# Kernel optimization log

Measured on AMD Instinct MI355X. Metric: run time of the kernel, lower is better.

Reference implementation:

```python
import jax, jax.numpy as jnp
import numpy as np

B, T, D, H, C, WIN = 2, 2048, 512, 8, 64, 128
EPS = 1e-6


def _rms_norm(x, w):
    # x: (..., C)
    norm = jax.lax.rsqrt(jnp.mean(x * x, axis=-1, keepdims=True) + EPS)
    return x * norm * w


def _apply_rope(x, cos_p, sin_p):
    # x: (B, H, T, C); cos_p/sin_p: (T, C)
    half = x.shape[-1] // 2
    x1, x2 = x[..., :half], x[..., half:]
    rotated = jnp.concatenate([-x2, x1], axis=-1)
    return x * cos_p + rotated * sin_p


def setup_inputs() -> dict:
    key = jax.random.key(0)
    ks = jax.random.split(key, 5)
    h = jax.random.normal(ks[0], (B, T, D), dtype=jnp.float32)
    # RoPE cache (rotate-half convention): (T_max, head_dim)
    inv_freq = 1.0 / (10000.0 ** (jnp.arange(0, C, 2, dtype=jnp.float32) / C))  # (C/2,)
    pos = jnp.arange(T, dtype=jnp.float32)
    freqs = pos[:, None] * inv_freq[None, :]                      # (T, C/2)
    emb = jnp.concatenate([freqs, freqs], axis=-1)                # (T, C)
    rope_cos = jnp.cos(emb)
    rope_sin = jnp.sin(emb)
    scale = 0.02
    W_q = jax.random.normal(ks[1], (D, H * C), dtype=jnp.float32) * scale
    W_k = jax.random.normal(ks[2], (D, H * C), dtype=jnp.float32) * scale
    W_v = jax.random.normal(ks[3], (D, H * C), dtype=jnp.float32) * scale
    W_o = jax.random.normal(ks[4], (H * C, D), dtype=jnp.float32) * scale
    q_norm_w = jnp.ones((C,), dtype=jnp.float32)
    k_norm_w = jnp.ones((C,), dtype=jnp.float32)
    return {"h": h, "rope_cos": rope_cos, "rope_sin": rope_sin,
            "W_q": W_q, "W_k": W_k, "W_v": W_v, "W_o": W_o,
            "q_norm_w": q_norm_w, "k_norm_w": k_norm_w}


def reference(h, rope_cos, rope_sin, W_q, W_k, W_v, W_o, q_norm_w, k_norm_w):
    Bx, Tx, _ = h.shape
    q = (h @ W_q).reshape(Bx, Tx, H, C)
    k = (h @ W_k).reshape(Bx, Tx, H, C)
    v = (h @ W_v).reshape(Bx, Tx, H, C)
    q = _rms_norm(q, q_norm_w)
    k = _rms_norm(k, k_norm_w)
    positions = jnp.arange(Tx)
    cos_p = rope_cos[positions]   # (T, C)
    sin_p = rope_sin[positions]
    # transpose to (B, H, T, C), apply rope, transpose back handled implicitly
    q = _apply_rope(q.transpose(0, 2, 1, 3), cos_p, sin_p).transpose(0, 2, 1, 3)
    k = _apply_rope(k.transpose(0, 2, 1, 3), cos_p, sin_p).transpose(0, 2, 1, 3)
    i = positions[:, None]
    j = positions[None, :]
    sw_mask = (j <= i) & (j > i - WIN)                # (T, T) banded causal
    logits = jnp.einsum('bthc,bshc->bhts', q, k) / np.sqrt(C).astype(np.float32)
    logits = jnp.where(sw_mask[None, None], logits, jnp.float32(-jnp.inf))
    attn = jax.nn.softmax(logits, axis=-1)
    out = jnp.einsum('bhts,bshc->bthc', attn, v).reshape(Bx, Tx, H * C)
    return out @ W_o
```

## Files before the change

### kernel.cpp

```cpp
#include <hip/hip_runtime.h>
#include <hip/hip_bf16.h>
#include <cmath>

#define Bb 2
#define Tt 2048
#define Dd 512
#define Hh 8
#define Cc 64
#define WINw 128

using u16x8 = __attribute__((ext_vector_type(8))) unsigned short;
using s16x8 = __attribute__((ext_vector_type(8))) short;
using f32x4 = __attribute__((ext_vector_type(4))) float;

__device__ __forceinline__ float bf2f(unsigned short u) {
  union { unsigned int i; float f; } v; v.i = ((unsigned int)u) << 16; return v.f;
}
__device__ __forceinline__ unsigned short f2bf(float f) {
  __hip_bfloat16 b = __float2bfloat16(f);
  return *reinterpret_cast<unsigned short*>(&b);
}

#define GLD16(gp, lp)                                                        \
  __builtin_amdgcn_global_load_lds(                                          \
      (const __attribute__((address_space(1))) unsigned int*)(gp),           \
      (__attribute__((address_space(3))) unsigned int*)(lp), 16, 0, 0)

__global__ __launch_bounds__(256) void prep_all(
    const float* __restrict__ s0, const float* __restrict__ s1,
    const float* __restrict__ s2, const float* __restrict__ s3,
    unsigned short* __restrict__ d,
    const float* __restrict__ hsrc, unsigned short* __restrict__ hdst) {
  int tid = threadIdx.x;
  if (blockIdx.z == 4) {
    int gid = ((int)blockIdx.y * 8 + blockIdx.x) * 256 + tid;
    #pragma unroll
    for (int s = 0; s < 16; ++s) {
      size_t i = ((size_t)s * 16384 + gid) * 8;
      const float4* g = (const float4*)&hsrc[i];
      float4 f0 = g[0], f1 = g[1];
      u16x8 o = {f2bf(f0.x), f2bf(f0.y), f2bf(f0.z), f2bf(f0.w),
                 f2bf(f1.x), f2bf(f1.y), f2bf(f1.z), f2bf(f1.w)};
      *(u16x8*)&hdst[i] = o;
    }
    return;
  }
  __shared__ unsigned short tile[64 * 65];
  const float* srcs[4] = {s0, s1, s2, s3};
  const float* src = srcs[blockIdx.z];
  unsigned short* dst = d + (size_t)blockIdx.z * 512 * 512;
  int n0 = blockIdx.x * 64, k0 = blockIdx.y * 64;
  int tx = tid & 63, ty = tid >> 6;
  #pragma unroll
  for (int i = 0; i < 16; ++i) {
    int k = ty * 16 + i;
    tile[k * 65 + tx] = f2bf(src[(k0 + k) * 512 + n0 + tx]);
  }
  __syncthreads();
  #pragma unroll
  for (int i = 0; i < 16; ++i) {
    int n = ty * 16 + i;
    dst[(n0 + n) * 512 + k0 + tx] = tile[tx * 65 + n];
  }
}

__global__ __launch_bounds__(256) void qkv_fused(
    const unsigned short* __restrict__ Hb,
    const unsigned short* __restrict__ WTall,
    const float* __restrict__ qnw, const float* __restrict__ knw,
    const float* __restrict__ rcos, const float* __restrict__ rsin,
    unsigned short* __restrict__ Qw, unsigned short* __restrict__ Kw,
    unsigned short* __restrict__ Vw) {
  __shared__ alignas(16) unsigned short Al[128 * 64];
  __shared__ alignas(16) unsigned short Bl[128 * 64];
  int tid = threadIdx.x;
  int wave = tid >> 6, lane = tid & 63;
  int ln = lane & 15, qd = lane >> 4;
  int wm = wave >> 1, wn = wave & 1;
  int m0 = blockIdx.x * 128, n0 = blockIdx.y * 128;

  f32x4 acc[4][4];
  #pragma unroll
  for (int mi = 0; mi < 4; ++mi)
    #pragma unroll
    for (int ni = 0; ni < 4; ++ni) acc[mi][ni] = f32x4{0.f, 0.f, 0.f, 0.f};

  for (int k0 = 0; k0 < 512; k0 += 64) {
    #pragma unroll
    for (int s = 0; s < 4; ++s) {
      int q = s * 4 + wave;
      int L = q * 64 + lane;
      int row = L >> 3;
      int cb = (L & 7) ^ (row & 7);
      const unsigned short* ga = &Hb[(size_t)(m0 + row) * 512 + k0 + cb * 8];
      GLD16(ga, (char*)Al + q * 1024);
      const unsigned short* gb = &WTall[(size_t)(n0 + row) * 512 + k0 + cb * 8];
      GLD16(gb, (char*)Bl + q * 1024);
    }
    __syncthreads();
    #pragma unroll
    for (int half = 0; half < 2; ++half) {
      s16x8 af[4], bfr[4];
      #pragma unroll
      for (int mi = 0; mi < 4; ++mi) {
        int ar = wm * 64 + mi * 16 + ln;
        int cbp = (qd + half * 4) ^ (ar & 7);
        af[mi] = *(const s16x8*)((const char*)Al + ar * 128 + cbp * 16);
      }
      #pragma unroll
      for (int ni = 0; ni < 4; ++ni) {
        int br = wn * 64 + ni * 16 + ln;
        int cbp = (qd + half * 4) ^ (br & 7);
        bfr[ni] = *(const s16x8*)((const char*)Bl + br * 128 + cbp * 16);
      }
      #pragma unroll
      for (int mi = 0; mi < 4; ++mi)
        #pragma unroll
        for (int ni = 0; ni < 4; ++ni)
          acc[mi][ni] = __builtin_amdgcn_mfma_f32_16x16x32_bf16(
              af[mi], bfr[ni], acc[mi][ni], 0, 0, 0);
    }
    __syncthreads();
  }

  int gh = blockIdx.y * 2 + wn;
  int mat = gh >> 3, head = gh & 7;
  unsigned short* Out = (mat == 0) ? Qw : (mat == 1) ? Kw : Vw;
  const float* nw = (mat == 0) ? qnw : knw;
  bool do_rope = (mat < 2);

  #pragma unroll
  for (int mi = 0; mi < 4; ++mi) {
    float vals[4][4];
    #pragma unroll
    for (int ni = 0; ni < 4; ++ni)
      #pragma unroll
      for (int r = 0; r < 4; ++r) vals[ni][r] = acc[mi][ni][r];

    if (do_rope) {
      #pragma unroll
      for (int r = 0; r < 4; ++r) {
        float ss = 0.f;
        #pragma unroll
        for (int ni = 0; ni < 4; ++ni) ss += vals[ni][r] * vals[ni][r];
        ss += __shfl_xor(ss, 1, 64);
        ss += __shfl_xor(ss, 2, 64);
        ss += __shfl_xor(ss, 4, 64);
        ss += __shfl_xor(ss, 8, 64);
        float nrm = rsqrtf(ss * (1.0f / 64.0f) + 1e-6f);
        #pragma unroll
        for (int ni = 0; ni < 4; ++ni) vals[ni][r] *= nrm;
      }
      #pragma unroll
      for (int ni = 0; ni < 4; ++ni) {
        float w = nw[ni * 16 + ln];
        #pragma unroll
        for (int r = 0; r < 4; ++r) vals[ni][r] *= w;
      }
      float res[4][4];
      #pragma unroll
      for (int r = 0; r < 4; ++r) {
        int row = m0 + wm * 64 + mi * 16 + qd * 4 + r;
        int t = row & (Tt - 1);
        #pragma unroll
        for (int ni = 0; ni < 4; ++ni) {
          int c = ni * 16 + ln;
          float cs = rcos[t * 64 + c];
          float sn = rsin[t * 64 + c];
          float part = vals[ni ^ 2][r];
          float rot = (ni < 2) ? -part : part;
          res[ni][r] = vals[ni][r] * cs + rot * sn;
        }
      }
      #pragma unroll
      for (int ni = 0; ni < 4; ++ni)
        #pragma unroll
        for (int r = 0; r < 4; ++r) vals[ni][r] = res[ni][r];
    }

    #pragma unroll
    for (int r = 0; r < 4; ++r) {
      int row = m0 + wm * 64 + mi * 16 + qd * 4 + r;
      int b = row >> 11, t = row & (Tt - 1);
      unsigned short* op = &Out[(((size_t)b * Hh + head) * Tt + t) * 64 + ln];
      #pragma unroll
      for (int ni = 0; ni < 4; ++ni) op[ni * 16] = f2bf(vals[ni][r]);
    }
  }
}

__global__ __launch_bounds__(256) void attn_mfma(
    const unsigned short* __restrict__ Q,
    const unsigned short* __restrict__ K,
    const unsigned short* __restrict__ V,
    unsigned short* __restrict__ AO) {
  __shared__ alignas(16) unsigned short Ql[64 * 72];
  __shared__ alignas(16) unsigned short KP[192 * 72];
  __shared__ alignas(16) unsigned short Vt[64 * 200];

  int tid = threadIdx.x;
  int wave = tid >> 6, lane = tid & 63;
  int ln = lane & 15, qd = lane >> 4;
  int qtile = blockIdx.x, bh = blockIdx.y;
  int t0 = qtile * 64;
  int kb = t0 - 128;

  const unsigned short* Qg = Q + ((size_t)bh * Tt + t0) * 64;
  const unsigned short* Kg = K + (size_t)bh * Tt * 64;
  const unsigned short* Vg = V + (size_t)bh * Tt * 64;

  int srow = tid >> 2;
  int scol = (tid & 3) * 16;

  {
    const u16x8* g = (const u16x8*)&Qg[srow * 64 + scol];
    u16x8 a0 = g[0], a1 = g[1];
    *(u16x8*)&Ql[srow * 72 + scol] = a0;
    *(u16x8*)&Ql[srow * 72 + scol + 8] = a1;
  }
  #pragma unroll
  for (int p = 0; p < 3; ++p) {
    int row = p * 64 + srow;
    int kg = kb + row; if (kg < 0) kg = 0;
    const u16x8* gk = (const u16x8*)&Kg[kg * 64 + scol];
    u16x8 k0 = gk[0], k1 = gk[1];
    const u16x8* gv = (const u16x8*)&Vg[kg * 64 + scol];
    u16x8 v0 = gv[0], v1 = gv[1];
    *(u16x8*)&KP[row * 72 + scol] = k0;
    *(u16x8*)&KP[row * 72 + scol + 8] = k1;
    #pragma unroll
    for (int j = 0; j < 8; ++j) {
      Vt[(scol + j) * 200 + row] = v0[j];
      Vt[(scol + 8 + j) * 200 + row] = v1[j];
    }
  }
  __syncthreads();

  int q0 = wave * 16;
  s16x8 aq0 = *(const s16x8*)&Ql[(q0 + ln) * 72 + qd * 8];
  s16x8 aq1 = *(const s16x8*)&Ql[(q0 + ln) * 72 + 32 + qd * 8];
  f32x4 sf[12];
  #pragma unroll
  for (int nt = 0; nt < 12; ++nt) {
    s16x8 b0 = *(const s16x8*)&KP[(nt * 16 + ln) * 72 + qd * 8];
    s16x8 b1 = *(const s16x8*)&KP[(nt * 16 + ln) * 72 + 32 + qd * 8];
    f32x4 acc = {0.f, 0.f, 0.f, 0.f};
    acc = __builtin_amdgcn_mfma_f32_16x16x32_bf16(aq0, b0, acc, 0, 0, 0);
    acc = __builtin_amdgcn_mfma_f32_16x16x32_bf16(aq1, b1, acc, 0, 0, 0);
    sf[nt] = acc;
  }
  __syncthreads();

  unsigned short* Pl = KP;
  int ok0 = (t0 < 128) ? (128 - t0) : 0;
  #pragma unroll
  for (int r = 0; r < 4; ++r) {
    int lq = q0 + qd * 4 + r;
    float mx = -INFINITY;
    #pragma unroll
    for (int nt = 0; nt < 12; ++nt) {
      int kk = nt * 16 + ln;
      bool valid = (kk > lq) && (kk <= lq + 128) && (kk >= ok0);
      float s = valid ? sf[nt][r] * 0.125f : -INFINITY;
      sf[nt][r] = s;
      mx = fmaxf(mx, s);
    }
    mx = fmaxf(mx, __shfl_xor(mx, 1, 64));
    mx = fmaxf(mx, __shfl_xor(mx, 2, 64));
    mx = fmaxf(mx, __shfl_xor(mx, 4, 64));
    mx = fmaxf(mx, __shfl_xor(mx, 8, 64));
    float sum = 0.f;
    #pragma unroll
    for (int nt = 0; nt < 12; ++nt) {
      float e = __expf(sf[nt][r] - mx);
      sf[nt][r] = e;
      sum += e;
    }
    sum += __shfl_xor(sum, 1, 64);
    sum += __shfl_xor(sum, 2, 64);
    sum += __shfl_xor(sum, 4, 64);
    sum += __shfl_xor(sum, 8, 64);
    float inv = 1.0f / sum;
    #pragma unroll
    for (int nt = 0; nt < 12; ++nt)
      Pl[lq * 200 + nt * 16 + ln] = f2bf(sf[nt][r] * inv);
  }
  __syncthreads();

  f32x4 oa[4] = {f32x4{0,0,0,0}, f32x4{0,0,0,0}, f32x4{0,0,0,0}, f32x4{0,0,0,0}};
  #pragma unroll
  for (int s = 0; s < 6; ++s) {
    s16x8 ap = *(const s16x8*)&Pl[(q0 + ln) * 200 + s * 32 + qd * 8];
    #pragma unroll
    for (int nt = 0; nt < 4; ++nt) {
      s16x8 bv = *(const s16x8*)&Vt[(nt * 16 + ln) * 200 + s * 32 + qd * 8];
      oa[nt] = __builtin_amdgcn_mfma_f32_16x16x32_bf16(ap, bv, oa[nt], 0, 0, 0);
    }
  }

  int b = bh >> 3, h = bh & 7;
  #pragma unroll
  for (int r = 0; r < 4; ++r) {
    int t = t0 + q0 + qd * 4 + r;
    unsigned short* op = &AO[(((size_t)b * Tt + t) * Hh + h) * 64 + ln];
    #pragma unroll
    for (int nt = 0; nt < 4; ++nt) op[nt * 16] = f2bf(oa[nt][r]);
  }
}

__global__ __launch_bounds__(256) void out_gemm(
    const unsigned short* __restrict__ Am,
    const unsigned short* __restrict__ WT,
    float* __restrict__ Out) {
  __shared__ alignas(16) unsigned short Al[64 * 64];
  __shared__ alignas(16) unsigned short Bl[128 * 64];
  int tid = threadIdx.x;
  int wave = tid >> 6, lane = tid & 63;
  int ln = lane & 15, qd = lane >> 4;
  int wm = wave >> 1, wn = wave & 1;
  int m0 = blockIdx.x * 64, n0 = blockIdx.y * 128;

  f32x4 acc[2][4];
  #pragma unroll
  for (int mi = 0; mi < 2; ++mi)
    #pragma unroll
    for (int ni = 0; ni < 4; ++ni) acc[mi][ni] = f32x4{0.f, 0.f, 0.f, 0.f};

  for (int k0 = 0; k0 < 512; k0 += 64) {
    #pragma unroll
    for (int s = 0; s < 2; ++s) {
      int q = s * 4 + wave;
      int L = q * 64 + lane;
      int row = L >> 3;
      int cb = (L & 7) ^ (row & 7);
      const unsigned short* ga = &Am[(size_t)(m0 + row) * 512 + k0 + cb * 8];
      GLD16(ga, (char*)Al + q * 1024);
    }
    #pragma unroll
    for (int s = 0; s < 4; ++s) {
      int q = s * 4 + wave;
      int L = q * 64 + lane;
      int row = L >> 3;
      int cb = (L & 7) ^ (row & 7);
      const unsigned short* gb = &WT[(size_t)(n0 + row) * 512 + k0 + cb * 8];
      GLD16(gb, (char*)Bl + q * 1024);
    }
    __syncthreads();
    #pragma unroll
    for (int half = 0; half < 2; ++half) {
      s16x8 af[2], bfr[4];
      #pragma unroll
      for (int mi = 0; mi < 2; ++mi) {
        int ar = wm * 32 + mi * 16 + ln;
        int cbp = (qd + half * 4) ^ (ar & 7);
        af[mi] = *(const s16x8*)((const char*)Al + ar * 128 + cbp * 16);
      }
      #pragma unroll
      for (int ni = 0; ni < 4; ++ni) {
        int br = wn * 64 + ni * 16 + ln;
        int cbp = (qd + half * 4) ^ (br & 7);
        bfr[ni] = *(const s16x8*)((const char*)Bl + br * 128 + cbp * 16);
      }
      #pragma unroll
      for (int mi = 0; mi < 2; ++mi)
        #pragma unroll
        for (int ni = 0; ni < 4; ++ni)
          acc[mi][ni] = __builtin_amdgcn_mfma_f32_16x16x32_bf16(
              af[mi], bfr[ni], acc[mi][ni], 0, 0, 0);
    }
    __syncthreads();
  }

  #pragma unroll
  for (int mi = 0; mi < 2; ++mi)
    #pragma unroll
    for (int r = 0; r < 4; ++r) {
      int row = m0 + wm * 32 + mi * 16 + qd * 4 + r;
      #pragma unroll
      for (int ni = 0; ni < 4; ++ni)
        Out[(size_t)row * 512 + n0 + wn * 64 + ni * 16 + ln] = acc[mi][ni][r];
    }
}

extern "C" void kernel_launch(void* const* d_in, const int* in_sizes, int n_in,
                              void* d_out, int out_size, void* d_ws, size_t ws_size,
                              hipStream_t stream) {
  const float* h   = (const float*)d_in[0];
  const float* rc  = (const float*)d_in[1];
  const float* rs  = (const float*)d_in[2];
  const float* Wq  = (const float*)d_in[3];
  const float* Wk  = (const float*)d_in[4];
  const float* Wv  = (const float*)d_in[5];
  const float* Wo  = (const float*)d_in[6];
  const float* qnw = (const float*)d_in[7];
  const float* knw = (const float*)d_in[8];

  unsigned short* ws    = (unsigned short*)d_ws;
  unsigned short* WTall = ws;
  unsigned short* WTo   = WTall + 1536 * 512;
  unsigned short* Hb    = WTo + 512 * 512;
  unsigned short* Qw    = Hb + 2097152;
  unsigned short* Kw    = Qw + 2097152;
  unsigned short* Vw    = Kw + 2097152;
  unsigned short* AOw   = Vw + 2097152;

  prep_all<<<dim3(8, 8, 5), 256, 0, stream>>>(Wq, Wk, Wv, Wo, WTall, h, Hb);

  qkv_fused<<<dim3(32, 12), 256, 0, stream>>>(Hb, WTall, qnw, knw, rc, rs,
                                              Qw, Kw, Vw);

  attn_mfma<<<dim3(32, 16), 256, 0, stream>>>(Qw, Kw, Vw, AOw);

  out_gemm<<<dim3(64, 4), 256, 0, stream>>>(AOw, WTo, (float*)d_out);
}
```

Before: 114.1 us.

## Store V transposed and stage QKV/attention outputs through LDS for coalesced writes

The QKV epilogue now writes each wave's 64x64 tile into shared memory and then issues 16-byte coalesced global stores. V is written pre-transposed as (C, T) per head, so the attention kernel can fill its Vt tile with vector loads instead of a scalar transpose scatter. The attention kernel also loads Q fragments straight from global memory, drops one barrier, and stages its output through LDS for vectorized stores. The V loads for the first query tiles no longer clamp negative key indices, so they can read before the buffer start; those positions are masked, but non-finite garbage would still poison the result.

```diff
diff --git a/kernel.cpp b/kernel.cpp
--- a/kernel.cpp
+++ b/kernel.cpp
@@ -71,8 +71,9 @@
     const float* __restrict__ rcos, const float* __restrict__ rsin,
     unsigned short* __restrict__ Qw, unsigned short* __restrict__ Kw,
     unsigned short* __restrict__ Vw) {
-  __shared__ alignas(16) unsigned short Al[128 * 64];
-  __shared__ alignas(16) unsigned short Bl[128 * 64];
+  __shared__ alignas(16) unsigned short S[18432];
+  unsigned short* Al = S;
+  unsigned short* Bl = S + 8192;
   int tid = threadIdx.x;
   int wave = tid >> 6, lane = tid & 63;
   int ln = lane & 15, qd = lane >> 4;
@@ -92,10 +93,8 @@
       int L = q * 64 + lane;
       int row = L >> 3;
       int cb = (L & 7) ^ (row & 7);
-      const unsigned short* ga = &Hb[(size_t)(m0 + row) * 512 + k0 + cb * 8];
-      GLD16(ga, (char*)Al + q * 1024);
-      const unsigned short* gb = &WTall[(size_t)(n0 + row) * 512 + k0 + cb * 8];
-      GLD16(gb, (char*)Bl + q * 1024);
+      GLD16(&Hb[(size_t)(m0 + row) * 512 + k0 + cb * 8], (char*)Al + q * 1024);
+      GLD16(&WTall[(size_t)(n0 + row) * 512 + k0 + cb * 8], (char*)Bl + q * 1024);
     }
     __syncthreads();
     #pragma unroll
@@ -123,11 +122,13 @@
     __syncthreads();
   }
 
+  unsigned short* Wl = S + wave * 4608;
   int gh = blockIdx.y * 2 + wn;
   int mat = gh >> 3, head = gh & 7;
-  unsigned short* Out = (mat == 0) ? Qw : (mat == 1) ? Kw : Vw;
   const float* nw = (mat == 0) ? qnw : knw;
   bool do_rope = (mat < 2);
+  int mrow0 = m0 + wm * 64;
+  int b = mrow0 >> 11, tb = mrow0 & (Tt - 1);
 
   #pragma unroll
   for (int mi = 0; mi < 4; ++mi) {
@@ -160,8 +161,7 @@
       float res[4][4];
       #pragma unroll
       for (int r = 0; r < 4; ++r) {
-        int row = m0 + wm * 64 + mi * 16 + qd * 4 + r;
-        int t = row & (Tt - 1);
+        int t = (tb + mi * 16 + qd * 4 + r);
         #pragma unroll
         for (int ni = 0; ni < 4; ++ni) {
           int c = ni * 16 + ln;
@@ -178,13 +178,37 @@
         for (int r = 0; r < 4; ++r) vals[ni][r] = res[ni][r];
     }
 
-    #pragma unroll
-    for (int r = 0; r < 4; ++r) {
-      int row = m0 + wm * 64 + mi * 16 + qd * 4 + r;
-      int b = row >> 11, t = row & (Tt - 1);
-      unsigned short* op = &Out[(((size_t)b * Hh + head) * Tt + t) * 64 + ln];
-      #pragma unroll
-      for (int ni = 0; ni < 4; ++ni) op[ni * 16] = f2bf(vals[ni][r]);
+    if (mat < 2) {
+      #pragma unroll
+      for (int ni = 0; ni < 4; ++ni)
+        #pragma unroll
+        for (int r = 0; r < 4; ++r)
+          Wl[(mi * 16 + qd * 4 + r) * 72 + ni * 16 + ln] = f2bf(vals[ni][r]);
+    } else {
+      #pragma unroll
+      for (int ni = 0; ni < 4; ++ni)
+        #pragma unroll
+        for (int r = 0; r < 4; ++r)
+          Wl[(ni * 16 + ln) * 72 + mi * 16 + qd * 4 + r] = f2bf(vals[ni][r]);
+    }
+  }
+
+  if (mat < 2) {
+    unsigned short* Og =
+        ((mat == 0) ? Qw : Kw) + (((size_t)b * Hh + head) * Tt + tb) * 64;
+    #pragma unroll
+    for (int i = 0; i < 8; ++i) {
+      int idx = i * 64 + lane;
+      int rr = idx >> 3, cc = (idx & 7) * 8;
+      *(u16x8*)&Og[rr * 64 + cc] = *(const u16x8*)&Wl[rr * 72 + cc];
+    }
+  } else {
+    unsigned short* Og = Vw + (((size_t)b * Hh + head) * 64) * 2048 + tb;
+    #pragma unroll
+    for (int i = 0; i < 8; ++i) {
+      int idx = i * 64 + lane;
+      int rr = idx >> 3, cc = (idx & 7) * 8;
+      *(u16x8*)&Og[(size_t)rr * 2048 + cc] = *(const u16x8*)&Wl[rr * 72 + cc];
     }
   }
 }
@@ -192,62 +216,53 @@
 __global__ __launch_bounds__(256) void attn_mfma(
     const unsigned short* __restrict__ Q,
     const unsigned short* __restrict__ K,
-    const unsigned short* __restrict__ V,
+    const unsigned short* __restrict__ Vg,
     unsigned short* __restrict__ AO) {
-  __shared__ alignas(16) unsigned short Ql[64 * 72];
   __shared__ alignas(16) unsigned short KP[192 * 72];
   __shared__ alignas(16) unsigned short Vt[64 * 200];
-
   int tid = threadIdx.x;
   int wave = tid >> 6, lane = tid & 63;
   int ln = lane & 15, qd = lane >> 4;
-  int qtile = blockIdx.x, bh = blockIdx.y;
-  int t0 = qtile * 64;
+  int t0 = blockIdx.x * 64, bh = blockIdx.y;
   int kb = t0 - 128;
-
-  const unsigned short* Qg = Q + ((size_t)bh * Tt + t0) * 64;
+  int q0 = wave * 16;
+
   const unsigned short* Kg = K + (size_t)bh * Tt * 64;
-  const unsigned short* Vg = V + (size_t)bh * Tt * 64;
-
-  int srow = tid >> 2;
-  int scol = (tid & 3) * 16;
-
-  {
-    const u16x8* g = (const u16x8*)&Qg[srow * 64 + scol];
-    u16x8 a0 = g[0], a1 = g[1];
-    *(u16x8*)&Ql[srow * 72 + scol] = a0;
-    *(u16x8*)&Ql[srow * 72 + scol + 8] = a1;
-  }
+  const unsigned short* Vb = Vg + (size_t)bh * 64 * 2048;
+
+  int srow = tid >> 2, scol = (tid & 3) * 16;
   #pragma unroll
   for (int p = 0; p < 3; ++p) {
     int row = p * 64 + srow;
     int kg = kb + row; if (kg < 0) kg = 0;
-    const u16x8* gk = (const u16x8*)&Kg[kg * 64 + scol];
-    u16x8 k0 = gk[0], k1 = gk[1];
-    const u16x8* gv = (const u16x8*)&Vg[kg * 64 + scol];
-    u16x8 v0 = gv[0], v1 = gv[1];
-    *(u16x8*)&KP[row * 72 + scol] = k0;
-    *(u16x8*)&KP[row * 72 + scol + 8] = k1;
-    #pragma unroll
-    for (int j = 0; j < 8; ++j) {
-      Vt[(scol + j) * 200 + row] = v0[j];
-      Vt[(scol + 8 + j) * 200 + row] = v1[j];
-    }
-  }
+    const u16x8* gk = (const u16x8*)&Kg[(size_t)kg * 64 + scol];
+    u16x8 k0v = gk[0], k1v = gk[1];
+    *(u16x8*)&KP[row * 72 + scol] = k0v;
+    *(u16x8*)&KP[row * 72 + scol + 8] = k1v;
+  }
+  #pragma unroll
+  for (int j = 0; j < 3; ++j)
+    #pragma unroll
+    for (int it = 0; it < 2; ++it) {
+      int idx = it * 256 + tid;
+      int row = idx >> 3, ch = (idx & 7) * 8;
+      u16x8 v = *(const u16x8*)&Vb[(size_t)row * 2048 + kb + j * 64 + ch];
+      *(u16x8*)&Vt[row * 200 + j * 64 + ch] = v;
+    }
+  const unsigned short* Qg = Q + ((size_t)bh * Tt + t0 + q0) * 64;
+  s16x8 aq0 = *(const s16x8*)&Qg[ln * 64 + qd * 8];
+  s16x8 aq1 = *(const s16x8*)&Qg[ln * 64 + 32 + qd * 8];
   __syncthreads();
 
-  int q0 = wave * 16;
-  s16x8 aq0 = *(const s16x8*)&Ql[(q0 + ln) * 72 + qd * 8];
-  s16x8 aq1 = *(const s16x8*)&Ql[(q0 + ln) * 72 + 32 + qd * 8];
   f32x4 sf[12];
   #pragma unroll
   for (int nt = 0; nt < 12; ++nt) {
     s16x8 b0 = *(const s16x8*)&KP[(nt * 16 + ln) * 72 + qd * 8];
     s16x8 b1 = *(const s16x8*)&KP[(nt * 16 + ln) * 72 + 32 + qd * 8];
-    f32x4 acc = {0.f, 0.f, 0.f, 0.f};
-    acc = __builtin_amdgcn_mfma_f32_16x16x32_bf16(aq0, b0, acc, 0, 0, 0);
-    acc = __builtin_amdgcn_mfma_f32_16x16x32_bf16(aq1, b1, acc, 0, 0, 0);
-    sf[nt] = acc;
+    f32x4 a = {0.f, 0.f, 0.f, 0.f};
+    a = __builtin_amdgcn_mfma_f32_16x16x32_bf16(aq0, b0, a, 0, 0, 0);
+    a = __builtin_amdgcn_mfma_f32_16x16x32_bf16(aq1, b1, a, 0, 0, 0);
+    sf[nt] = a;
   }
   __syncthreads();
 
@@ -285,7 +300,6 @@
     for (int nt = 0; nt < 12; ++nt)
       Pl[lq * 200 + nt * 16 + ln] = f2bf(sf[nt][r] * inv);
   }
-  __syncthreads();
 
   f32x4 oa[4] = {f32x4{0,0,0,0}, f32x4{0,0,0,0}, f32x4{0,0,0,0}, f32x4{0,0,0,0}};
   #pragma unroll
@@ -298,13 +312,19 @@
     }
   }
 
+  unsigned short* Ow = KP + q0 * 200;
+  #pragma unroll
+  for (int ni = 0; ni < 4; ++ni)
+    #pragma unroll
+    for (int r = 0; r < 4; ++r)
+      Ow[(qd * 4 + r) * 72 + ni * 16 + ln] = f2bf(oa[ni][r]);
   int b = bh >> 3, h = bh & 7;
   #pragma unroll
-  for (int r = 0; r < 4; ++r) {
-    int t = t0 + q0 + qd * 4 + r;
-    unsigned short* op = &AO[(((size_t)b * Tt + t) * Hh + h) * 64 + ln];
-    #pragma unroll
-    for (int nt = 0; nt < 4; ++nt) op[nt * 16] = f2bf(oa[nt][r]);
+  for (int i = 0; i < 2; ++i) {
+    int idx = i * 64 + lane;
+    int rr = idx >> 3, cc = (idx & 7) * 8;
+    *(u16x8*)&AO[((size_t)(b * Tt + t0 + q0 + rr) * Hh + h) * 64 + cc] =
+        *(const u16x8*)&Ow[rr * 72 + cc];
   }
 }
 
@@ -333,8 +353,7 @@
       int L = q * 64 + lane;
       int row = L >> 3;
       int cb = (L & 7) ^ (row & 7);
-      const unsigned short* ga = &Am[(size_t)(m0 + row) * 512 + k0 + cb * 8];
-      GLD16(ga, (char*)Al + q * 1024);
+      GLD16(&Am[(size_t)(m0 + row) * 512 + k0 + cb * 8], (char*)Al + q * 1024);
     }
     #pragma unroll
     for (int s = 0; s < 4; ++s) {
@@ -342,8 +361,7 @@
       int L = q * 64 + lane;
       int row = L >> 3;
       int cb = (L & 7) ^ (row & 7);
-      const unsigned short* gb = &WT[(size_t)(n0 + row) * 512 + k0 + cb * 8];
-      GLD16(gb, (char*)Bl + q * 1024);
+      GLD16(&WT[(size_t)(n0 + row) * 512 + k0 + cb * 8], (char*)Bl + q * 1024);
     }
     __syncthreads();
     #pragma unroll
```

After: 113.7 us. No clear change (-0.3%).
